# Optimization experiments

Hardware: AMD Instinct MI355X
Metric: run time of the kernel (lower is better)

The kernel has to match this reference:

```python
import jax, jax.numpy as jnp
import numpy as np

FP8_E4M3_MAX = 448.0

def fp8_quant_dequant(x):
    # Per-tensor dynamic scaling to e4m3 range, round-trip through fp8.
    amax = jnp.max(jnp.abs(x))
    scale = FP8_E4M3_MAX / jnp.maximum(amax, 1e-12)
    xq = (x * scale).astype(jnp.float8_e4m3fn).astype(x.dtype) / scale
    return xq

def fp8_linear(x, w, b):
    # quantize activations and weights to fp8, GEMM in the compute dtype, add bias
    return jnp.matmul(fp8_quant_dequant(x), fp8_quant_dequant(w)) + b

def setup_inputs() -> dict:
    key = jax.random.key(0)
    k1, k2, k3 = jax.random.split(key, 3)
    M, D_IN, D_H, D_OUT = 8192, 4096, 16384, 4096
    x = jax.random.normal(k1, (M, D_IN), dtype=jnp.float32)
    w1 = jax.random.normal(k2, (D_IN, D_H), dtype=jnp.float32)
    b1 = jnp.zeros((D_H,), dtype=jnp.float32)
    w2 = jax.random.normal(k3, (D_H, D_OUT), dtype=jnp.float32)
    b2 = jnp.zeros((D_OUT,), dtype=jnp.float32)
    return {"x": x, "w1": w1, "b1": b1, "w2": w2, "b2": b2}

def reference(x, w1, b1, w2, b2):
    h = jax.nn.relu(fp8_linear(x, w1, b1))
    return fp8_linear(h, w2, b2)
```

## Files before the change

kernel.cpp:

```cpp
#include <hip/hip_runtime.h>
#include <stdint.h>

typedef float f32x4 __attribute__((ext_vector_type(4)));
typedef int v4i __attribute__((ext_vector_type(4)));
typedef int v8i __attribute__((ext_vector_type(8)));

#define FP8MAX 448.0f

__device__ __forceinline__ float amax_scale(float amax) {
    return FP8MAX / fmaxf(amax, 1e-12f);
}

__global__ void amax_kernel(const float* __restrict__ x, long n, float* __restrict__ out) {
    long idx = (long)blockIdx.x * blockDim.x + threadIdx.x;
    long stride = (long)gridDim.x * blockDim.x;
    float m = 0.0f;
    for (long j = idx * 4; j < n; j += stride * 4) {
        f32x4 v = *(const f32x4*)(x + j);
        m = fmaxf(m, fmaxf(fmaxf(__builtin_fabsf(v.x), __builtin_fabsf(v.y)),
                           fmaxf(__builtin_fabsf(v.z), __builtin_fabsf(v.w))));
    }
#pragma unroll
    for (int o = 32; o > 0; o >>= 1) m = fmaxf(m, __shfl_xor(m, o, 64));
    if ((threadIdx.x & 63) == 0) atomicMax((int*)out, __float_as_int(m));
}

__global__ void quant_kernel(const float* __restrict__ x, uint8_t* __restrict__ q,
                             const float* __restrict__ amaxp, long n) {
    const float s = amax_scale(*amaxp);
    long idx = (long)blockIdx.x * blockDim.x + threadIdx.x;
    long stride = (long)gridDim.x * blockDim.x;
    for (long j = idx * 4; j < n; j += stride * 4) {
        f32x4 v = *(const f32x4*)(x + j);
        int p0 = __builtin_amdgcn_cvt_pk_fp8_f32(v.x * s, v.y * s, 0, false);
        int p1 = __builtin_amdgcn_cvt_pk_fp8_f32(v.z * s, v.w * s, 0, false);
        *(uint32_t*)(q + j) = (uint32_t)(p0 & 0xffff) | ((uint32_t)p1 << 16);
    }
}

__global__ void quant_transpose_kernel(const float* __restrict__ w, uint8_t* __restrict__ wqT,
                                       const float* __restrict__ amaxp, int R, int C) {
    __shared__ float tile[32][33];
    const float sc = amax_scale(*amaxp);
    const int col0 = blockIdx.x * 32;
    const int row0 = blockIdx.y * 32;
    const int tx = threadIdx.x & 31;
    const int ty = threadIdx.x >> 5;
#pragma unroll
    for (int i = 0; i < 4; i++)
        tile[ty + i * 8][tx] = w[(long)(row0 + ty + i * 8) * C + col0 + tx];
    __syncthreads();
    const int c  = threadIdx.x >> 3;
    const int kk = (threadIdx.x & 7) * 4;
    float v0 = tile[kk + 0][c] * sc, v1 = tile[kk + 1][c] * sc;
    float v2 = tile[kk + 2][c] * sc, v3 = tile[kk + 3][c] * sc;
    int p0 = __builtin_amdgcn_cvt_pk_fp8_f32(v0, v1, 0, false);
    int p1 = __builtin_amdgcn_cvt_pk_fp8_f32(v2, v3, 0, false);
    *(uint32_t*)(wqT + (long)(col0 + c) * R + row0 + kk) =
        (uint32_t)(p0 & 0xffff) | ((uint32_t)p1 << 16);
}

__device__ __forceinline__ void lds_dma16(const void* g, void* l) {
    __builtin_amdgcn_global_load_lds((__attribute__((address_space(1))) void*)(void*)g,
                                     (__attribute__((address_space(3))) void*)l, 16, 0, 0);
}

template <bool RELU, bool AMAX>
__global__ __launch_bounds__(512, 2) void gemm_mxfp8_kernel(
    const uint8_t* __restrict__ A, const uint8_t* __restrict__ Bt,
    float* __restrict__ C, const float* __restrict__ bias,
    const float* __restrict__ amaxA, const float* __restrict__ amaxB,
    float* __restrict__ amaxOut, int M, int N, int K) {
    __shared__ __align__(16) uint8_t As[2][256 * 128];
    __shared__ __align__(16) uint8_t Bs[2][256 * 128];

    const int t = threadIdx.x;
    const int lane = t & 63;
    const int wave = t >> 6;
    const int wm = wave >> 2;
    const int wn = wave & 3;

    int bid = (int)blockIdx.x;
    bid = (bid & 7) * ((int)gridDim.x >> 3) + (bid >> 3);
    const int nbn = N >> 8;
    const int bm = bid / nbn;
    const int bn = bid - bm * nbn;

    const int rs = t >> 3;
    const int us = (t & 7) ^ (rs & 7);
    const uint8_t* ag = A + (long)(bm * 256 + rs) * K + us * 16;
    const uint8_t* bg = Bt + (long)(bn * 256 + rs) * K + us * 16;

    auto stage = [&](int buf, int kt) {
        const uint8_t* a_ = ag + (long)kt * 128;
        const uint8_t* b_ = bg + (long)kt * 128;
        uint8_t* al_ = &As[buf][t * 16];
        uint8_t* bl_ = &Bs[buf][t * 16];
#pragma unroll
        for (int d = 0; d < 4; d++) {
            lds_dma16(a_ + (long)d * 64 * K, al_ + d * 8192);
            lds_dma16(b_ + (long)d * 64 * K, bl_ + d * 8192);
        }
    };

    const int lrow = lane & 15;
    const int g = lane >> 4;
    const int x7 = lane & 7;
    const int u0 = ((2 * g + 0) ^ x7) * 16;
    const int u1 = ((2 * g + 1) ^ x7) * 16;
    const int roA = (wm * 128 + lrow) * 128;
    const int roB = (wn * 64 + lrow) * 128;

    f32x4 acc[8][4] = {};
    const int NT = K >> 7;

    stage(0, 0);
    asm volatile("s_waitcnt vmcnt(0)" ::: "memory");
    __builtin_amdgcn_s_barrier();
    asm volatile("" ::: "memory");

    for (int kt = 0; kt < NT; ++kt) {
        const int b = kt & 1;
        const uint8_t* Ab = As[b];
        const uint8_t* Bb = Bs[b];
        if (kt + 1 < NT) stage(b ^ 1, kt + 1);

        v8i bf[4];
#pragma unroll
        for (int j = 0; j < 4; j++) {
            const uint8_t* p = Bb + roB + j * 2048;
            *(v4i*)&bf[j] = *(const v4i*)(p + u0);
            *((v4i*)&bf[j] + 1) = *(const v4i*)(p + u1);
        }
#pragma unroll
        for (int ph = 0; ph < 4; ph++) {
            v8i a0, a1;
            const uint8_t* pa0 = Ab + roA + (2 * ph + 0) * 2048;
            const uint8_t* pa1 = Ab + roA + (2 * ph + 1) * 2048;
            *(v4i*)&a0 = *(const v4i*)(pa0 + u0);
            *((v4i*)&a0 + 1) = *(const v4i*)(pa0 + u1);
            *(v4i*)&a1 = *(const v4i*)(pa1 + u0);
            *((v4i*)&a1 + 1) = *(const v4i*)(pa1 + u1);
            __builtin_amdgcn_s_barrier();
            __builtin_amdgcn_s_setprio(1);
#pragma unroll
            for (int j = 0; j < 4; j++) {
                acc[2 * ph + 0][j] = __builtin_amdgcn_mfma_scale_f32_16x16x128_f8f6f4(
                    a0, bf[j], acc[2 * ph + 0][j], 0, 0,
                    0, 0x7f7f7f7f, 0, 0x7f7f7f7f);
                acc[2 * ph + 1][j] = __builtin_amdgcn_mfma_scale_f32_16x16x128_f8f6f4(
                    a1, bf[j], acc[2 * ph + 1][j], 0, 0,
                    0, 0x7f7f7f7f, 0, 0x7f7f7f7f);
            }
            __builtin_amdgcn_s_setprio(0);
            if (ph == 3) {
                asm volatile("s_waitcnt vmcnt(0)" ::: "memory");
            }
            __builtin_amdgcn_s_barrier();
            if (ph == 3) asm volatile("" ::: "memory");
        }
    }

    const float inv = 1.0f / (amax_scale(*amaxA) * amax_scale(*amaxB));
    const int rg = (lane >> 4) * 4;
    const int cl = lane & 15;
    const int orow = bm * 256 + wm * 128 + rg;
    const int ocol = bn * 256 + wn * 64 + cl;
    float lmax = 0.0f;
#pragma unroll
    for (int j = 0; j < 4; j++) {
        const float bv = bias[ocol + j * 16];
#pragma unroll
        for (int i = 0; i < 8; i++) {
#pragma unroll
            for (int r = 0; r < 4; r++) {
                float v = acc[i][j][r] * inv + bv;
                if (RELU) v = fmaxf(v, 0.0f);
                C[(long)(orow + i * 16 + r) * N + ocol + j * 16] = v;
                if (AMAX) lmax = fmaxf(lmax, __builtin_fabsf(v));
            }
        }
    }
    if (AMAX) {
#pragma unroll
        for (int o = 32; o > 0; o >>= 1) lmax = fmaxf(lmax, __shfl_xor(lmax, o, 64));
        if (lane == 0) atomicMax((int*)amaxOut, __float_as_int(lmax));
    }
}

extern "C" void kernel_launch(void* const* d_in, const int* in_sizes, int n_in,
                              void* d_out, int out_size, void* d_ws, size_t ws_size,
                              hipStream_t stream) {
    const float* x  = (const float*)d_in[0];
    const float* w1 = (const float*)d_in[1];
    const float* b1 = (const float*)d_in[2];
    const float* w2 = (const float*)d_in[3];
    const float* b2 = (const float*)d_in[4];
    float* out = (float*)d_out;

    const int N1 = in_sizes[2];
    const int N2 = in_sizes[4];
    const int K1 = in_sizes[1] / N1;
    const int M  = in_sizes[0] / K1;

    uint8_t* ws = (uint8_t*)d_ws;
    float* amax_x  = (float*)(ws + 0);
    float* amax_w1 = (float*)(ws + 4);
    float* amax_w2 = (float*)(ws + 8);
    float* amax_h  = (float*)(ws + 12);
    size_t off = 256;
    uint8_t* xq   = ws + off; off += (size_t)M * K1;
    uint8_t* w1qT = ws + off; off += (size_t)K1 * N1;
    uint8_t* w2qT = ws + off; off += (size_t)N1 * N2;
    uint8_t* hq   = ws + off; off += (size_t)M * N1;
    float*   h    = (float*)(ws + off); off += (size_t)M * N1 * 4;

    hipMemsetAsync(d_ws, 0, 256, stream);

    amax_kernel<<<1024, 256, 0, stream>>>(x,  (long)M * K1,  amax_x);
    amax_kernel<<<1024, 256, 0, stream>>>(w1, (long)K1 * N1, amax_w1);
    amax_kernel<<<1024, 256, 0, stream>>>(w2, (long)N1 * N2, amax_w2);

    quant_kernel<<<2048, 256, 0, stream>>>(x, xq, amax_x, (long)M * K1);
    quant_transpose_kernel<<<dim3(N1 / 32, K1 / 32), 256, 0, stream>>>(w1, w1qT, amax_w1, K1, N1);
    quant_transpose_kernel<<<dim3(N2 / 32, N1 / 32), 256, 0, stream>>>(w2, w2qT, amax_w2, N1, N2);

    gemm_mxfp8_kernel<true, true><<<(M / 256) * (N1 / 256), 512, 0, stream>>>(
        xq, w1qT, h, b1, amax_x, amax_w1, amax_h, M, N1, K1);

    quant_kernel<<<4096, 256, 0, stream>>>(h, hq, amax_h, (long)M * N1);

    gemm_mxfp8_kernel<false, false><<<(M / 256) * (N2 / 256), 512, 0, stream>>>(
        hq, w2qT, out, b2, amax_h, amax_w2, nullptr, M, N2, N1);
}
```

Before: 2.582 ms.

## Spread next-tile LDS DMA prefetch across MFMA phases with partial vmcnt waits

The next k-tile's global-to-LDS copies are split into per-chunk issues. B chunks are issued in phase 0 and A chunks in phases 1 and 2, instead of all at once at the top of the iteration. The full vmcnt(0) drain becomes partial waits (vmcnt(6) after phase 1, vmcnt(2) after phase 3), so the A row-chunks needed only in later phases can still be in flight into the next iteration. The aim is to interleave memory traffic with MFMA work and reduce stalls at the tile boundary. In exchange, the last iteration issues a redundant prefetch, and correctness now depends on precise counter bookkeeping.

```diff
diff --git a/kernel.cpp b/kernel.cpp
--- a/kernel.cpp
+++ b/kernel.cpp
@@ -91,16 +91,11 @@
     const uint8_t* ag = A + (long)(bm * 256 + rs) * K + us * 16;
     const uint8_t* bg = Bt + (long)(bn * 256 + rs) * K + us * 16;
 
-    auto stage = [&](int buf, int kt) {
-        const uint8_t* a_ = ag + (long)kt * 128;
-        const uint8_t* b_ = bg + (long)kt * 128;
-        uint8_t* al_ = &As[buf][t * 16];
-        uint8_t* bl_ = &Bs[buf][t * 16];
-#pragma unroll
-        for (int d = 0; d < 4; d++) {
-            lds_dma16(a_ + (long)d * 64 * K, al_ + d * 8192);
-            lds_dma16(b_ + (long)d * 64 * K, bl_ + d * 8192);
-        }
+    auto stA = [&](int buf, int kt, int d) {
+        lds_dma16(ag + (long)kt * 128 + (long)d * 64 * K, &As[buf][t * 16 + d * 8192]);
+    };
+    auto stB = [&](int buf, int kt, int d) {
+        lds_dma16(bg + (long)kt * 128 + (long)d * 64 * K, &Bs[buf][t * 16 + d * 8192]);
     };
 
     const int lrow = lane & 15;
@@ -114,52 +109,64 @@
     f32x4 acc[8][4] = {};
     const int NT = K >> 7;
 
-    stage(0, 0);
-    asm volatile("s_waitcnt vmcnt(0)" ::: "memory");
+    stB(0, 0, 0); stB(0, 0, 1); stB(0, 0, 2); stB(0, 0, 3);
+    stA(0, 0, 0); stA(0, 0, 2);
+    stA(0, 0, 1); stA(0, 0, 3);
+    asm volatile("s_waitcnt vmcnt(2)" ::: "memory");
     __builtin_amdgcn_s_barrier();
     asm volatile("" ::: "memory");
 
     for (int kt = 0; kt < NT; ++kt) {
         const int b = kt & 1;
-        const uint8_t* Ab = As[b];
-        const uint8_t* Bb = Bs[b];
-        if (kt + 1 < NT) stage(b ^ 1, kt + 1);
+        const int nb = b ^ 1;
+        const uint8_t* __restrict__ Ab = &As[b][0];
+        const uint8_t* __restrict__ Bb = &Bs[b][0];
+        const int ktn = (kt + 1 < NT) ? kt + 1 : NT - 1;
 
         v8i bf[4];
 #pragma unroll
-        for (int j = 0; j < 4; j++) {
-            const uint8_t* p = Bb + roB + j * 2048;
-            *(v4i*)&bf[j] = *(const v4i*)(p + u0);
-            *((v4i*)&bf[j] + 1) = *(const v4i*)(p + u1);
-        }
-#pragma unroll
-        for (int ph = 0; ph < 4; ph++) {
+        for (int p = 0; p < 4; ++p) {
+            if (p == 0) {
+#pragma unroll
+                for (int j = 0; j < 4; ++j) {
+                    const uint8_t* q = Bb + roB + j * 2048;
+                    *(v4i*)&bf[j] = *(const v4i*)(q + u0);
+                    *((v4i*)&bf[j] + 1) = *(const v4i*)(q + u1);
+                }
+            }
             v8i a0, a1;
-            const uint8_t* pa0 = Ab + roA + (2 * ph + 0) * 2048;
-            const uint8_t* pa1 = Ab + roA + (2 * ph + 1) * 2048;
-            *(v4i*)&a0 = *(const v4i*)(pa0 + u0);
-            *((v4i*)&a0 + 1) = *(const v4i*)(pa0 + u1);
-            *(v4i*)&a1 = *(const v4i*)(pa1 + u0);
-            *((v4i*)&a1 + 1) = *(const v4i*)(pa1 + u1);
+            {
+                const uint8_t* pa0 = Ab + roA + (2 * p + 0) * 2048;
+                const uint8_t* pa1 = Ab + roA + (2 * p + 1) * 2048;
+                *(v4i*)&a0 = *(const v4i*)(pa0 + u0);
+                *((v4i*)&a0 + 1) = *(const v4i*)(pa0 + u1);
+                *(v4i*)&a1 = *(const v4i*)(pa1 + u0);
+                *((v4i*)&a1 + 1) = *(const v4i*)(pa1 + u1);
+            }
+            if (p == 0)      { stB(nb, ktn, 0); stB(nb, ktn, 1); stB(nb, ktn, 2); stB(nb, ktn, 3); }
+            else if (p == 1) { stA(nb, ktn, 0); stA(nb, ktn, 2); }
+            else if (p == 2) { stA(nb, ktn, 1); stA(nb, ktn, 3); }
+            asm volatile("" ::: "memory");
             __builtin_amdgcn_s_barrier();
             __builtin_amdgcn_s_setprio(1);
 #pragma unroll
-            for (int j = 0; j < 4; j++) {
-                acc[2 * ph + 0][j] = __builtin_amdgcn_mfma_scale_f32_16x16x128_f8f6f4(
-                    a0, bf[j], acc[2 * ph + 0][j], 0, 0,
+            for (int j = 0; j < 4; ++j) {
+                acc[2 * p + 0][j] = __builtin_amdgcn_mfma_scale_f32_16x16x128_f8f6f4(
+                    a0, bf[j], acc[2 * p + 0][j], 0, 0,
                     0, 0x7f7f7f7f, 0, 0x7f7f7f7f);
-                acc[2 * ph + 1][j] = __builtin_amdgcn_mfma_scale_f32_16x16x128_f8f6f4(
-                    a1, bf[j], acc[2 * ph + 1][j], 0, 0,
+                acc[2 * p + 1][j] = __builtin_amdgcn_mfma_scale_f32_16x16x128_f8f6f4(
+                    a1, bf[j], acc[2 * p + 1][j], 0, 0,
                     0, 0x7f7f7f7f, 0, 0x7f7f7f7f);
             }
             __builtin_amdgcn_s_setprio(0);
-            if (ph == 3) {
-                asm volatile("s_waitcnt vmcnt(0)" ::: "memory");
-            }
+            if (p == 1) asm volatile("s_waitcnt vmcnt(6)" ::: "memory");
+            if (p == 3) asm volatile("s_waitcnt vmcnt(2)" ::: "memory");
+            asm volatile("" ::: "memory");
             __builtin_amdgcn_s_barrier();
-            if (ph == 3) asm volatile("" ::: "memory");
+            asm volatile("" ::: "memory");
         }
     }
+    asm volatile("s_waitcnt vmcnt(0)" ::: "memory");
 
     const float inv = 1.0f / (amax_scale(*amaxA) * amax_scale(*amaxB));
     const int rg = (lane >> 4) * 4;
```

Measured after the change: 2.381 ms. 7.8% less time.
